# Performance work log

Measured on AMD Instinct MI355X. Metric: run time of the kernel, lower is better.

Reference implementation:

```python
import jax, jax.numpy as jnp
import numpy as np

D_MODEL = 2048
NUM_HEADS = 16
D_H = D_MODEL // NUM_HEADS
D_LATENT = 512
B, S = 2, 2048


def setup_inputs() -> dict:
    key = jax.random.key(0)
    ks = jax.random.split(key, 10)
    sd = lambda fan_in: 1.0 / np.sqrt(fan_in)
    x = jax.random.normal(ks[0], (B, S, D_MODEL), dtype=jnp.float32)
    # weights stored as [in, out] so y = x @ W + b (same math as nn.Linear)
    w_latent = jax.random.uniform(ks[1], (D_MODEL, D_LATENT), jnp.float32, -sd(D_MODEL), sd(D_MODEL))
    b_latent = jax.random.uniform(ks[2], (D_LATENT,), jnp.float32, -sd(D_MODEL), sd(D_MODEL))
    w_q = jax.random.uniform(ks[3], (D_MODEL, D_MODEL), jnp.float32, -sd(D_MODEL), sd(D_MODEL))
    b_q = jax.random.uniform(ks[4], (D_MODEL,), jnp.float32, -sd(D_MODEL), sd(D_MODEL))
    # per-head K/V projections batched into [H, d_latent, d_h]
    w_k = jax.random.uniform(ks[5], (NUM_HEADS, D_LATENT, D_H), jnp.float32, -sd(D_LATENT), sd(D_LATENT))
    b_k = jax.random.uniform(ks[6], (NUM_HEADS, D_H), jnp.float32, -sd(D_LATENT), sd(D_LATENT))
    w_v = jax.random.uniform(ks[7], (NUM_HEADS, D_LATENT, D_H), jnp.float32, -sd(D_LATENT), sd(D_LATENT))
    b_v = jax.random.uniform(ks[8], (NUM_HEADS, D_H), jnp.float32, -sd(D_LATENT), sd(D_LATENT))
    w_o = jax.random.uniform(ks[9], (D_MODEL, D_MODEL), jnp.float32, -sd(D_MODEL), sd(D_MODEL))
    b_o = jnp.zeros((D_MODEL,), jnp.float32)
    return {"x": x, "w_latent": w_latent, "b_latent": b_latent, "w_q": w_q, "b_q": b_q,
            "w_k": w_k, "b_k": b_k, "w_v": w_v, "b_v": b_v, "w_o": w_o, "b_o": b_o}


def reference(x, w_latent, b_latent, w_q, b_q, w_k, b_k, w_v, b_v, w_o, b_o):
    batch, seq, d = x.shape
    # latent KV compression: [B,S,d_latent]
    z = x @ w_latent + b_latent
    # queries: [B,H,S,d_h]
    q = (x @ w_q + b_q).reshape(batch, seq, NUM_HEADS, D_H).transpose(0, 2, 1, 3)
    # per-head K/V projections fused into one batched GEMM: [B,H,S,d_h]
    k = jnp.einsum('bsl,hld->bhsd', z, w_k) + b_k[None, :, None, :]
    v = jnp.einsum('bsl,hld->bhsd', z, w_v) + b_v[None, :, None, :]
    attn = jnp.einsum('bhqd,bhkd->bhqk', q, k) / np.sqrt(D_H).astype(np.float32)
    attn = jax.nn.softmax(attn, axis=-1)
    out = jnp.einsum('bhqk,bhkd->bhqd', attn, v)          # [B,H,S,d_h]
    out = out.transpose(0, 2, 1, 3).reshape(batch, seq, d)  # [B,S,D]
    return out @ w_o + b_o
```

## Files before the change

kernel.cpp:

```cpp
#include <hip/hip_runtime.h>
#include <hip/hip_bf16.h>

#define H_ATT   16
#define DH      128
#define DMODEL  2048
#define DLAT    512
#define NB      2
#define SEQ     2048
#define MROWS   (NB * SEQ)
#define NQZ     (DMODEL + DLAT)
#define NKV     (2 * DMODEL)

#define SCL2 0.12751744f

typedef __bf16          bf16x8_t __attribute__((ext_vector_type(8)));
typedef float           f32x4_t  __attribute__((ext_vector_type(4)));
typedef unsigned short  u16x4_t  __attribute__((ext_vector_type(4)));

#if __has_builtin(__builtin_amdgcn_exp2f)
#define EXP2F(x) __builtin_amdgcn_exp2f(x)
#else
#define EXP2F(x) exp2f(x)
#endif

__device__ __forceinline__ unsigned short f2bf_u16(float f) {
  union { __bf16 b; unsigned short u; } cv; cv.b = (__bf16)f; return cv.u;
}

__device__ __forceinline__ void async_copy16(const __bf16* g, __bf16* l) {
  __builtin_amdgcn_global_load_lds(
      (const __attribute__((address_space(1))) unsigned int*)g,
      (__attribute__((address_space(3))) unsigned int*)l, 16, 0, 0);
}

#define NB_CAST 8192
#define NB_WQ   4096
#define NB_WL   1024
#define NB_WK   1024
#define NB_WV   1024
#define NB_WO   4096
#define NB_BIAS 26
#define NB_PREP (NB_CAST + NB_WQ + NB_WL + NB_WK + NB_WV + NB_WO + NB_BIAS)

__global__ void prep(const float* __restrict__ x,
                     const float* __restrict__ w_q, const float* __restrict__ w_latent,
                     const float* __restrict__ w_k, const float* __restrict__ w_v,
                     const float* __restrict__ w_o,
                     const float* __restrict__ b_q, const float* __restrict__ b_lat,
                     const float* __restrict__ b_k, const float* __restrict__ b_v,
                     __bf16* __restrict__ xb, __bf16* __restrict__ wqzt,
                     __bf16* __restrict__ wkvt, __bf16* __restrict__ wot,
                     float* __restrict__ bqz, float* __restrict__ bkv) {
  __shared__ float tile[32][33];
  int bi = blockIdx.x;
  int t  = threadIdx.x;

  if (bi < NB_CAST) {
    int i = bi * 256 + t;
    float4 v = ((const float4*)x)[i];
    ushort4 o;
    o.x = f2bf_u16(v.x); o.y = f2bf_u16(v.y); o.z = f2bf_u16(v.z); o.w = f2bf_u16(v.w);
    ((ushort4*)xb)[i] = o;
    return;
  }
  bi -= NB_CAST;

  const float* in = nullptr; __bf16* out = nullptr;
  int R = 0, C = 0, bx = 0, by = 0; float scale = 1.f;
  if (bi < NB_WQ) {
    in = w_q; out = wqzt; R = DMODEL; C = DMODEL; scale = SCL2;
    bx = bi & 63; by = bi >> 6;
  } else if ((bi -= NB_WQ) < NB_WL) {
    in = w_latent; out = wqzt + (size_t)DMODEL * DMODEL; R = DMODEL; C = DLAT;
    bx = bi & 15; by = bi >> 4;
  } else if ((bi -= NB_WL) < NB_WK) {
    int h = bi >> 6, rem = bi & 63;
    in = w_k + (size_t)h * DLAT * DH; out = wkvt + (size_t)h * DH * DLAT;
    R = DLAT; C = DH; bx = rem & 3; by = rem >> 2;
  } else if ((bi -= NB_WK) < NB_WV) {
    int h = bi >> 6, rem = bi & 63;
    in = w_v + (size_t)h * DLAT * DH;
    out = wkvt + (size_t)DMODEL * DLAT + (size_t)h * DH * DLAT;
    R = DLAT; C = DH; bx = rem & 3; by = rem >> 2;
  } else if ((bi -= NB_WV) < NB_WO) {
    in = w_o; out = wot; R = DMODEL; C = DMODEL;
    bx = bi & 63; by = bi >> 6;
  } else {
    bi -= NB_WO;
    int idx = bi * 256 + t;
    if (idx < DMODEL)                bqz[idx] = b_q[idx] * SCL2;
    else if (idx < NQZ)              bqz[idx] = b_lat[idx - DMODEL];
    else if (idx < NQZ + DMODEL)     bkv[idx - NQZ] = b_k[idx - NQZ];
    else if (idx < NQZ + NKV)        bkv[idx - NQZ] = b_v[idx - NQZ - DMODEL];
    return;
  }

  int tx = t & 31, ty = t >> 5;
  const float* ip = in + (size_t)(by * 32) * C + bx * 32;
  #pragma unroll
  for (int i = 0; i < 4; ++i)
    tile[ty + i * 8][tx] = ip[(size_t)(ty + i * 8) * C + tx];
  __syncthreads();
  __bf16* op = out + (size_t)(bx * 32) * R + by * 32;
  #pragma unroll
  for (int i = 0; i < 4; ++i)
    op[(size_t)(ty + i * 8) * R + tx] = (__bf16)(tile[tx][ty + i * 8] * scale);
}

#define BM 128
#define BN 128
#define BK 32

__device__ __forceinline__ void storec(float*  p, float v) { *p = v; }
__device__ __forceinline__ void storec(__bf16* p, float v) { *p = (__bf16)v; }

template <typename OutT, bool KVDUAL>
__global__ __launch_bounds__(256, 3)
void gemm_bt(const __bf16* __restrict__ A, const __bf16* __restrict__ Bt,
             const float* __restrict__ bias, OutT* __restrict__ C,
             __bf16* __restrict__ Cvt,
             int M, int N, int K, int lda, int ldc) {
  __shared__ __align__(16) __bf16 As[BM * BK];
  __shared__ __align__(16) __bf16 Bs[BN * BK];
  const int t    = threadIdx.x;
  const int wave = t >> 6, lane = t & 63;
  const int quad = lane >> 4, l16 = lane & 15;
  const int wm = (wave >> 1) * 64, wn = (wave & 1) * 64;
  const int row0 = blockIdx.y * BM, col0 = blockIdx.x * BN;
  const int srow = t >> 2, skc = t & 3;

  const __bf16* Ag  = A  + (size_t)(row0 + srow)      * lda + skc * 8;
  const __bf16* Ag2 = A  + (size_t)(row0 + srow + 64) * lda + skc * 8;
  const __bf16* Bg  = Bt + (size_t)(col0 + srow)      * K   + skc * 8;
  const __bf16* Bg2 = Bt + (size_t)(col0 + srow + 64) * K   + skc * 8;
  __bf16* Al  = As + t * 8;
  __bf16* Al2 = As + 2048 + t * 8;
  __bf16* Bl  = Bs + t * 8;
  __bf16* Bl2 = Bs + 2048 + t * 8;

  f32x4_t acc[4][4] = {};

  for (int k0 = 0; k0 < K; k0 += BK) {
    async_copy16(Ag  + k0, Al);
    async_copy16(Ag2 + k0, Al2);
    async_copy16(Bg  + k0, Bl);
    async_copy16(Bg2 + k0, Bl2);
    __syncthreads();
    bf16x8_t af[4], bfr[4];
    #pragma unroll
    for (int i = 0; i < 4; ++i)
      af[i] = *(const bf16x8_t*)(As + (wm + i * 16 + l16) * BK + quad * 8);
    #pragma unroll
    for (int j = 0; j < 4; ++j)
      bfr[j] = *(const bf16x8_t*)(Bs + (wn + j * 16 + l16) * BK + quad * 8);
    #pragma unroll
    for (int i = 0; i < 4; ++i)
      #pragma unroll
      for (int j = 0; j < 4; ++j)
        acc[i][j] = __builtin_amdgcn_mfma_f32_16x16x32_bf16(af[i], bfr[j], acc[i][j], 0, 0, 0);
    __syncthreads();
  }

  const bool vmode = KVDUAL && (col0 >= DMODEL);
  #pragma unroll
  for (int j = 0; j < 4; ++j) {
    int col = col0 + wn + j * 16 + l16;
    float bj = bias[col];
    #pragma unroll
    for (int i = 0; i < 4; ++i) {
      int row = row0 + wm + i * 16 + quad * 4;
      if (vmode) {
        u16x4_t pw;
        #pragma unroll
        for (int r = 0; r < 4; ++r) pw[r] = f2bf_u16(acc[i][j][r] + bj);
        size_t bb = (size_t)(row >> 11);
        int s = row & (SEQ - 1);
        *(u16x4_t*)(Cvt + bb * ((size_t)DMODEL * SEQ) + (size_t)(col - DMODEL) * SEQ + s) = pw;
      } else {
        #pragma unroll
        for (int r = 0; r < 4; ++r)
          storec(&C[(size_t)(row + r) * ldc + col], acc[i][j][r] + bj);
      }
    }
  }
}

#define TQ 128
#define TK 64
#define NT (SEQ / TK)

__global__ __launch_bounds__(256, 2)
void mla_attn(const __bf16* __restrict__ Qm, const __bf16* __restrict__ Km,
              const __bf16* __restrict__ Vtg, __bf16* __restrict__ Om) {
  __shared__ __align__(16) __bf16 smem[5 * 16 * 512];
  __bf16* const Kls = smem;
  __bf16* const Vls = smem + 2 * (16 * 512);
  __bf16* const Ps  = smem + 4 * (16 * 512);
  float*  const Lbuf = (float*)smem;

  const int t    = threadIdx.x;
  const int wave = t >> 6, lane = t & 63;
  const int quad = lane >> 4, l16 = lane & 15;
  const int wq = wave >> 1, wk = wave & 1, wd = wave & 1;
  const int lin  = blockIdx.x;
  const int xcd  = lin & 7, slot = lin >> 3;
  const int hb   = xcd * 4 + (slot >> 4);
  const int b    = hb >> 4, h = hb & 15;
  const int q0   = (slot & 15) * TQ;
  const size_t kbase  = (size_t)b * SEQ * DMODEL + (size_t)h * DH;
  const size_t vtbase = ((size_t)b * DMODEL + (size_t)h * DH) * SEQ;
  const size_t obase  = (size_t)b * SEQ * DMODEL + (size_t)h * DH;

  bf16x8_t qf[4][4];
  #pragma unroll
  for (int nt = 0; nt < 4; ++nt) {
    const __bf16* qp = Qm + ((size_t)b * SEQ + q0 + wq * 64 + nt * 16 + l16) * NQZ
                       + (size_t)h * DH + quad * 8;
    #pragma unroll
    for (int kc = 0; kc < 4; ++kc)
      qf[nt][kc] = *(const bf16x8_t*)(qp + kc * 32);
  }

  auto stageK = [&](int kt0, int buf) {
    #pragma unroll
    for (int i2 = 0; i2 < 4; ++i2) {
      int bidx = wave * 4 + i2;
      int mt = bidx >> 2, kc = bidx & 3;
      async_copy16(Km + kbase + (size_t)(kt0 + mt * 16 + l16) * DMODEL + kc * 32 + quad * 8,
                   Kls + buf * (16 * 512) + bidx * 512 + lane * 8);
    }
  };
  auto stageV = [&](int kt0, int buf) {
    #pragma unroll
    for (int i2 = 0; i2 < 4; ++i2) {
      int bidx = wave * 4 + i2;
      int dt = bidx >> 1, ks = bidx & 1;
      async_copy16(Vtg + vtbase + (size_t)(dt * 16 + l16) * SEQ + kt0 + ks * 32 + quad * 8,
                   Vls + buf * (16 * 512) + bidx * 512 + lane * 8);
    }
  };

  f32x4_t acc_o[4][4] = {};
  float l_part[4] = {0.f, 0.f, 0.f, 0.f};

  stageK(0, 0);
  stageV(0, 0);

  f32x4_t acc_s[2][4];
  for (int it = 0; it < NT; ++it) {
    __syncthreads();

    if (it + 1 < NT) stageK((it + 1) * TK, (it + 1) & 1);

    if (it > 0) {
      const __bf16* Vb = Vls + ((it - 1) & 1) * (16 * 512);
      __builtin_amdgcn_s_setprio(1);
      #pragma unroll
      for (int ks = 0; ks < 2; ++ks) {
        bf16x8_t pf[4];
        #pragma unroll
        for (int mq = 0; mq < 4; ++mq)
          pf[mq] = *(const bf16x8_t*)(Ps + ((wq * 4 + mq) * 2 + ks) * 512 + lane * 8);
        #pragma unroll
        for (int nd = 0; nd < 4; ++nd) {
          bf16x8_t vf = *(const bf16x8_t*)(Vb + ((wd * 4 + nd) * 2 + ks) * 512 + lane * 8);
          #pragma unroll
          for (int mq = 0; mq < 4; ++mq)
            acc_o[mq][nd] = __builtin_amdgcn_mfma_f32_16x16x32_bf16(pf[mq], vf, acc_o[mq][nd], 0, 0, 0);
        }
      }
      __builtin_amdgcn_s_setprio(0);
    }

    #pragma unroll
    for (int mtl = 0; mtl < 2; ++mtl)
      #pragma unroll
      for (int nt = 0; nt < 4; ++nt)
        acc_s[mtl][nt] = f32x4_t{0.f, 0.f, 0.f, 0.f};
    const __bf16* Kb = Kls + (it & 1) * (16 * 512);
    __builtin_amdgcn_s_setprio(1);
    #pragma unroll
    for (int kc = 0; kc < 4; ++kc)
      #pragma unroll
      for (int mtl = 0; mtl < 2; ++mtl) {
        bf16x8_t kf = *(const bf16x8_t*)(Kb + ((wk * 2 + mtl) * 4 + kc) * 512 + lane * 8);
        #pragma unroll
        for (int nt = 0; nt < 4; ++nt)
          acc_s[mtl][nt] = __builtin_amdgcn_mfma_f32_16x16x32_bf16(kf, qf[nt][kc], acc_s[mtl][nt], 0, 0, 0);
      }
    __builtin_amdgcn_s_setprio(0);

    __builtin_amdgcn_s_barrier();

    if (it + 1 < NT) stageV((it + 1) * TK, (it + 1) & 1);

    #pragma unroll
    for (int nt = 0; nt < 4; ++nt) {
      #pragma unroll
      for (int mtl = 0; mtl < 2; ++mtl) {
        u16x4_t pw;
        float s = 0.f;
        #pragma unroll
        for (int r = 0; r < 4; ++r) {
          float p = EXP2F(fminf(acc_s[mtl][nt][r], 80.f));
          s += p;
          pw[r] = f2bf_u16(p);
        }
        l_part[nt] += s;
        *(u16x4_t*)(Ps + ((wq * 4 + nt) * 2 + wk) * 512
                    + ((mtl * 2 + (quad >> 1)) * 16 + l16) * 8 + (quad & 1) * 4) = pw;
      }
    }
  }

  __syncthreads();
  {
    const __bf16* Vb = Vls + ((NT - 1) & 1) * (16 * 512);
    __builtin_amdgcn_s_setprio(1);
    #pragma unroll
    for (int ks = 0; ks < 2; ++ks) {
      bf16x8_t pf[4];
      #pragma unroll
      for (int mq = 0; mq < 4; ++mq)
        pf[mq] = *(const bf16x8_t*)(Ps + ((wq * 4 + mq) * 2 + ks) * 512 + lane * 8);
      #pragma unroll
      for (int nd = 0; nd < 4; ++nd) {
        bf16x8_t vf = *(const bf16x8_t*)(Vb + ((wd * 4 + nd) * 2 + ks) * 512 + lane * 8);
        #pragma unroll
        for (int mq = 0; mq < 4; ++mq)
          acc_o[mq][nd] = __builtin_amdgcn_mfma_f32_16x16x32_bf16(pf[mq], vf, acc_o[mq][nd], 0, 0, 0);
      }
    }
    __builtin_amdgcn_s_setprio(0);
  }

  #pragma unroll
  for (int nt = 0; nt < 4; ++nt) {
    float lp = l_part[nt];
    lp += __shfl_xor(lp, 16);
    lp += __shfl_xor(lp, 32);
    Lbuf[wk * TQ + wq * 64 + nt * 16 + l16] = lp;
  }
  __syncthreads();
  #pragma unroll
  for (int mq = 0; mq < 4; ++mq) {
    float li[4];
    #pragma unroll
    for (int r = 0; r < 4; ++r) {
      int qq = wq * 64 + mq * 16 + quad * 4 + r;
      li[r] = 1.f / (Lbuf[0 * TQ + qq] + Lbuf[1 * TQ + qq]);
    }
    #pragma unroll
    for (int nd = 0; nd < 4; ++nd) {
      int col = wd * 64 + nd * 16 + l16;
      #pragma unroll
      for (int r = 0; r < 4; ++r) {
        int row = q0 + wq * 64 + mq * 16 + quad * 4 + r;
        Om[obase + (size_t)row * DMODEL + col] = (__bf16)(acc_o[mq][nd][r] * li[r]);
      }
    }
  }
}

extern "C" void kernel_launch(void* const* d_in, const int* in_sizes, int n_in,
                              void* d_out, int out_size, void* d_ws, size_t ws_size,
                              hipStream_t stream) {
  (void)in_sizes; (void)n_in; (void)out_size; (void)ws_size;
  const float* x        = (const float*)d_in[0];
  const float* w_latent = (const float*)d_in[1];
  const float* b_latent = (const float*)d_in[2];
  const float* w_q      = (const float*)d_in[3];
  const float* b_q      = (const float*)d_in[4];
  const float* w_k      = (const float*)d_in[5];
  const float* b_k      = (const float*)d_in[6];
  const float* w_v      = (const float*)d_in[7];
  const float* b_v      = (const float*)d_in[8];
  const float* w_o      = (const float*)d_in[9];
  const float* b_o      = (const float*)d_in[10];
  float* out = (float*)d_out;

  __bf16* ws = (__bf16*)d_ws;
  __bf16* xb   = ws; ws += (size_t)MROWS * DMODEL;
  __bf16* wqzt = ws; ws += (size_t)NQZ * DMODEL;
  __bf16* wkvt = ws; ws += (size_t)NKV * DLAT;
  __bf16* wot  = ws; ws += (size_t)DMODEL * DMODEL;
  __bf16* qzb  = ws; ws += (size_t)MROWS * NQZ;
  __bf16* kb   = ws; ws += (size_t)MROWS * DMODEL;
  __bf16* vt   = ws; ws += (size_t)MROWS * DMODEL;
  __bf16* ao   = ws; ws += (size_t)MROWS * DMODEL;
  float*  bqz  = (float*)ws;
  float*  bkv  = bqz + NQZ;

  dim3 blk256(256);
  prep<<<NB_PREP, blk256, 0, stream>>>(x, w_q, w_latent, w_k, w_v, w_o,
                                       b_q, b_latent, b_k, b_v,
                                       xb, wqzt, wkvt, wot, bqz, bkv);

  gemm_bt<__bf16, false><<<dim3(NQZ/BN, MROWS/BM), blk256, 0, stream>>>(
      xb, wqzt, bqz, qzb, nullptr, MROWS, NQZ, DMODEL, DMODEL, NQZ);
  gemm_bt<__bf16, true><<<dim3(NKV/BN, MROWS/BM), blk256, 0, stream>>>(
      qzb + DMODEL, wkvt, bkv, kb, vt, MROWS, NKV, DLAT, NQZ, DMODEL);

  mla_attn<<<dim3(512), blk256, 0, stream>>>(qzb, kb, vt, ao);

  gemm_bt<float, false><<<dim3(DMODEL/BN, MROWS/BM), blk256, 0, stream>>>(
      ao, wot, b_o, out, nullptr, MROWS, DMODEL, DMODEL, DMODEL, DMODEL);
}
```

Measured before the change: 340.5 us.

## Replace GEMM with 256x256 double-buffered 8-wave kernel and XCD-aware block remap

Replaces the 128x128x32 single-buffered GEMM with a 256x256x64 tile on 512 threads. Global-to-LDS copies are double-buffered and interleaved with the MFMA phases, using explicit vmcnt waits, barriers and setprio. Block indices are remapped across the 8 XCDs for better L2 locality. Larger tiles cut global traffic per FLOP and the pipelining hides load latency, at the cost of fewer blocks (e.g. 160/256/128 per GEMM), which may underfill 256 CUs, plus heavy register pressure from 32 accumulators per lane.

```diff
diff --git a/kernel.cpp b/kernel.cpp
--- a/kernel.cpp
+++ b/kernel.cpp
@@ -107,79 +107,130 @@
     op[(size_t)(ty + i * 8) * R + tx] = (__bf16)(tile[tx][ty + i * 8] * scale);
 }
 
-#define BM 128
-#define BN 128
-#define BK 32
+#define GBM 256
+#define GBN 256
+#define GBK 64
 
 __device__ __forceinline__ void storec(float*  p, float v) { *p = v; }
 __device__ __forceinline__ void storec(__bf16* p, float v) { *p = (__bf16)v; }
 
 template <typename OutT, bool KVDUAL>
-__global__ __launch_bounds__(256, 3)
-void gemm_bt(const __bf16* __restrict__ A, const __bf16* __restrict__ Bt,
+__global__ __launch_bounds__(512, 2)
+void gemm256(const __bf16* __restrict__ A, const __bf16* __restrict__ Bt,
              const float* __restrict__ bias, OutT* __restrict__ C,
              __bf16* __restrict__ Cvt,
-             int M, int N, int K, int lda, int ldc) {
-  __shared__ __align__(16) __bf16 As[BM * BK];
-  __shared__ __align__(16) __bf16 Bs[BN * BK];
+             int K, int lda, int ldb, int ldc, int gx) {
+  __shared__ __align__(16) __bf16 lds[4 * 16384];
   const int t    = threadIdx.x;
   const int wave = t >> 6, lane = t & 63;
   const int quad = lane >> 4, l16 = lane & 15;
-  const int wm = (wave >> 1) * 64, wn = (wave & 1) * 64;
-  const int row0 = blockIdx.y * BM, col0 = blockIdx.x * BN;
-  const int srow = t >> 2, skc = t & 3;
-
-  const __bf16* Ag  = A  + (size_t)(row0 + srow)      * lda + skc * 8;
-  const __bf16* Ag2 = A  + (size_t)(row0 + srow + 64) * lda + skc * 8;
-  const __bf16* Bg  = Bt + (size_t)(col0 + srow)      * K   + skc * 8;
-  const __bf16* Bg2 = Bt + (size_t)(col0 + srow + 64) * K   + skc * 8;
-  __bf16* Al  = As + t * 8;
-  __bf16* Al2 = As + 2048 + t * 8;
-  __bf16* Bl  = Bs + t * 8;
-  __bf16* Bl2 = Bs + 2048 + t * 8;
-
-  f32x4_t acc[4][4] = {};
-
-  for (int k0 = 0; k0 < K; k0 += BK) {
-    async_copy16(Ag  + k0, Al);
-    async_copy16(Ag2 + k0, Al2);
-    async_copy16(Bg  + k0, Bl);
-    async_copy16(Bg2 + k0, Bl2);
-    __syncthreads();
-    bf16x8_t af[4], bfr[4];
-    #pragma unroll
-    for (int i = 0; i < 4; ++i)
-      af[i] = *(const bf16x8_t*)(As + (wm + i * 16 + l16) * BK + quad * 8);
-    #pragma unroll
-    for (int j = 0; j < 4; ++j)
-      bfr[j] = *(const bf16x8_t*)(Bs + (wn + j * 16 + l16) * BK + quad * 8);
-    #pragma unroll
-    for (int i = 0; i < 4; ++i)
-      #pragma unroll
-      for (int j = 0; j < 4; ++j)
-        acc[i][j] = __builtin_amdgcn_mfma_f32_16x16x32_bf16(af[i], bfr[j], acc[i][j], 0, 0, 0);
-    __syncthreads();
+  const int WM = wave >> 2, WN = wave & 3;
+
+  const int nwg = gridDim.x;
+  const int lin = blockIdx.x;
+  const int wg  = (lin & 7) * (nwg >> 3) + (lin >> 3);
+  const int bx  = wg % gx, by = wg / gx;
+  const int row0 = by * GBM, col0 = bx * GBN;
+
+  const __bf16* Apb[2][2];
+  const __bf16* Bpb[2][2];
+  #pragma unroll
+  for (int h = 0; h < 2; ++h)
+    #pragma unroll
+    for (int r = 0; r < 2; ++r) {
+      int blk = r * 8 + wave;
+      int fi  = h * 8 + (blk >> 1);
+      int kc  = blk & 1;
+      Apb[h][r] = A  + (size_t)(row0 + fi * 16 + l16) * lda + kc * 32 + quad * 8;
+      Bpb[h][r] = Bt + (size_t)(col0 + fi * 16 + l16) * ldb + kc * 32 + quad * 8;
+    }
+
+  auto stageA = [&](int kt, int h, int buf) {
+    #pragma unroll
+    for (int r = 0; r < 2; ++r)
+      async_copy16(Apb[h][r] + (size_t)kt * GBK,
+                   lds + buf * 16384 + (h * 16 + r * 8 + wave) * 512 + lane * 8);
+  };
+  auto stageB = [&](int kt, int h, int buf) {
+    #pragma unroll
+    for (int r = 0; r < 2; ++r)
+      async_copy16(Bpb[h][r] + (size_t)kt * GBK,
+                   lds + 32768 + buf * 16384 + (h * 16 + r * 8 + wave) * 512 + lane * 8);
+  };
+
+  f32x4_t acc[8][4] = {};
+  const int NKT = K >> 6;
+
+  stageB(0, 0, 0); stageB(0, 1, 0);
+  stageA(0, 0, 0); stageA(0, 1, 0);
+  stageB(1, 0, 1); stageB(1, 1, 1);
+  asm volatile("s_waitcnt vmcnt(4)" ::: "memory");
+  __builtin_amdgcn_s_barrier();
+
+  for (int j = 0; j < NKT; ++j) {
+    const int cur = j & 1, nxt = cur ^ 1;
+    const __bf16* Ab = lds + cur * 16384;
+    const __bf16* Bb = lds + 32768 + cur * 16384;
+
+    bf16x8_t bfr[4][2];
+    #pragma unroll
+    for (int f = 0; f < 4; ++f)
+      #pragma unroll
+      for (int kc = 0; kc < 2; ++kc)
+        bfr[f][kc] = *(const bf16x8_t*)(Bb + ((WN * 4 + f) * 2 + kc) * 512 + lane * 8);
+
+    #pragma unroll
+    for (int p = 0; p < 4; ++p) {
+      bf16x8_t a[2][2];
+      #pragma unroll
+      for (int i = 0; i < 2; ++i)
+        #pragma unroll
+        for (int kc = 0; kc < 2; ++kc)
+          a[i][kc] = *(const bf16x8_t*)(Ab + ((WM * 8 + p * 2 + i) * 2 + kc) * 512 + lane * 8);
+
+      if (p == 0)      { if (j + 1 < NKT) stageA(j + 1, 0, nxt); }
+      else if (p == 1) { if (j + 1 < NKT) stageA(j + 1, 1, nxt); }
+      else if (p == 2) { if (j + 2 < NKT) stageB(j + 2, 0, cur); }
+      else             { if (j + 2 < NKT) stageB(j + 2, 1, cur); }
+
+      __builtin_amdgcn_s_barrier();
+      __builtin_amdgcn_s_setprio(1);
+      #pragma unroll
+      for (int kc = 0; kc < 2; ++kc)
+        #pragma unroll
+        for (int i = 0; i < 2; ++i)
+          #pragma unroll
+          for (int f = 0; f < 4; ++f)
+            acc[p * 2 + i][f] = __builtin_amdgcn_mfma_f32_16x16x32_bf16(
+                a[i][kc], bfr[f][kc], acc[p * 2 + i][f], 0, 0, 0);
+      __builtin_amdgcn_s_setprio(0);
+      if (p == 3) {
+        if (j + 2 < NKT) asm volatile("s_waitcnt vmcnt(4)" ::: "memory");
+        else             asm volatile("s_waitcnt vmcnt(0)" ::: "memory");
+      }
+      __builtin_amdgcn_s_barrier();
+    }
   }
 
   const bool vmode = KVDUAL && (col0 >= DMODEL);
   #pragma unroll
-  for (int j = 0; j < 4; ++j) {
-    int col = col0 + wn + j * 16 + l16;
+  for (int f = 0; f < 4; ++f) {
+    int col = col0 + WN * 64 + f * 16 + l16;
     float bj = bias[col];
     #pragma unroll
-    for (int i = 0; i < 4; ++i) {
-      int row = row0 + wm + i * 16 + quad * 4;
+    for (int mi = 0; mi < 8; ++mi) {
+      int row = row0 + WM * 128 + mi * 16 + quad * 4;
       if (vmode) {
         u16x4_t pw;
         #pragma unroll
-        for (int r = 0; r < 4; ++r) pw[r] = f2bf_u16(acc[i][j][r] + bj);
+        for (int r = 0; r < 4; ++r) pw[r] = f2bf_u16(acc[mi][f][r] + bj);
         size_t bb = (size_t)(row >> 11);
         int s = row & (SEQ - 1);
         *(u16x4_t*)(Cvt + bb * ((size_t)DMODEL * SEQ) + (size_t)(col - DMODEL) * SEQ + s) = pw;
       } else {
         #pragma unroll
         for (int r = 0; r < 4; ++r)
-          storec(&C[(size_t)(row + r) * ldc + col], acc[i][j][r] + bj);
+          storec(&C[(size_t)(row + r) * ldc + col], acc[mi][f][r] + bj);
       }
     }
   }
@@ -392,17 +443,18 @@
   float*  bkv  = bqz + NQZ;
 
   dim3 blk256(256);
+  dim3 blk512(512);
   prep<<<NB_PREP, blk256, 0, stream>>>(x, w_q, w_latent, w_k, w_v, w_o,
                                        b_q, b_latent, b_k, b_v,
                                        xb, wqzt, wkvt, wot, bqz, bkv);
 
-  gemm_bt<__bf16, false><<<dim3(NQZ/BN, MROWS/BM), blk256, 0, stream>>>(
-      xb, wqzt, bqz, qzb, nullptr, MROWS, NQZ, DMODEL, DMODEL, NQZ);
-  gemm_bt<__bf16, true><<<dim3(NKV/BN, MROWS/BM), blk256, 0, stream>>>(
-      qzb + DMODEL, wkvt, bkv, kb, vt, MROWS, NKV, DLAT, NQZ, DMODEL);
+  gemm256<__bf16, false><<<dim3((MROWS/GBM)*(NQZ/GBN)), blk512, 0, stream>>>(
+      xb, wqzt, bqz, qzb, nullptr, DMODEL, DMODEL, DMODEL, NQZ, NQZ/GBN);
+  gemm256<__bf16, true><<<dim3((MROWS/GBM)*(NKV/GBN)), blk512, 0, stream>>>(
+      qzb + DMODEL, wkvt, bkv, kb, vt, DLAT, NQZ, DLAT, DMODEL, NKV/GBN);
 
   mla_attn<<<dim3(512), blk256, 0, stream>>>(qzb, kb, vt, ao);
 
-  gemm_bt<float, false><<<dim3(DMODEL/BN, MROWS/BM), blk256, 0, stream>>>(
-      ao, wot, b_o, out, nullptr, MROWS, DMODEL, DMODEL, DMODEL, DMODEL);
-}
+  gemm256<float, false><<<dim3((MROWS/GBM)*(DMODEL/GBN)), blk512, 0, stream>>>(
+      ao, wot, b_o, out, nullptr, DMODEL, DMODEL, DMODEL, DMODEL, DMODEL/GBN);
+}
```

After: 363.8 us. 6.9% more time.
